# Kernel optimization log

Hardware: AMD Instinct MI355X
Metric: run time of the kernel (lower is better)

The kernel has to match this reference:

```python
import jax, jax.numpy as jnp
import numpy as np

N, M, D, DV = 8192, 8192, 64, 64

def setup_inputs() -> dict:
    key = jax.random.key(0)
    kq, kk, kv = jax.random.split(key, 3)
    Q = jax.random.normal(kq, (N, D), dtype=jnp.float32)
    K = jax.random.normal(kk, (M, D), dtype=jnp.float32)
    V = jax.random.normal(kv, (M, DV), dtype=jnp.float32)
    return {"Q": Q, "K": K, "V": V}

def reference(Q, K, V):
    d = K.shape[-1]
    scores = jnp.einsum('nd,md->nm', Q, K) / jnp.sqrt(jnp.float32(d))  # [N, M]
    attn = jax.nn.softmax(scores, axis=-1)
    return attn @ V  # [N, DV]
```

## Files before the change

### kernel.cpp

```cpp
#include <hip/hip_runtime.h>


#define NQ 8192
#define NK 8192

typedef float f32x4 __attribute__((ext_vector_type(4)));
typedef short short8 __attribute__((ext_vector_type(8)));
union U4 { uint4 u; short8 s; };

#define MFMA16 __builtin_amdgcn_mfma_f32_16x16x32_bf16

__device__ __forceinline__ unsigned pk2(float a, float b) {
    unsigned ua = __builtin_bit_cast(unsigned, a);
    unsigned ub = __builtin_bit_cast(unsigned, b);
    ua = (ua + 0x7FFFu + ((ua >> 16) & 1u)) >> 16;
    ub = (ub + 0x7FFFu + ((ub >> 16) & 1u)) & 0xFFFF0000u;
    return ua | ub;
}

__device__ __forceinline__ unsigned pkt(float a, float b) {
    return __builtin_amdgcn_perm(__builtin_bit_cast(unsigned, b),
                                 __builtin_bit_cast(unsigned, a), 0x07060302u);
}

__global__ __launch_bounds__(256)
void prepass(const float* __restrict__ Kg, const float* __restrict__ Vg,
             uint4* __restrict__ Kb4, uint4* __restrict__ Vt4) {
    __shared__ float ld[64 * 33];
    const int t = threadIdx.x, b = blockIdx.x;

    if (b < 256) {
        const int kl = t >> 3, dg = t & 7;
        const int e = kl & 1, i16 = kl >> 1, h = dg >> 2, q = dg & 3;
        const float* gp = Kg + (size_t)(b * 32 + kl) * 64 + dg * 8;
        float4 f0 = *(const float4*)gp;
        float4 f1 = *(const float4*)(gp + 4);
        uint4 o = make_uint4(pk2(f0.x, f0.y), pk2(f0.z, f0.w),
                             pk2(f1.x, f1.y), pk2(f1.z, f1.w));
        Kb4[(size_t)(b * 4 + e * 2 + h) * 64 + i16 * 4 + q] = o;
    } else {
        const int c = b - 256;
        {
            const int key = t >> 3, dg = t & 7;
            const float* gp = Vg + (size_t)(c * 32 + key) * 64 + dg * 8;
            float4 f0 = *(const float4*)gp;
            float4 f1 = *(const float4*)(gp + 4);
            ld[(dg * 8 + 0) * 33 + key] = f0.x;
            ld[(dg * 8 + 1) * 33 + key] = f0.y;
            ld[(dg * 8 + 2) * 33 + key] = f0.z;
            ld[(dg * 8 + 3) * 33 + key] = f0.w;
            ld[(dg * 8 + 4) * 33 + key] = f1.x;
            ld[(dg * 8 + 5) * 33 + key] = f1.y;
            ld[(dg * 8 + 6) * 33 + key] = f1.z;
            ld[(dg * 8 + 7) * 33 + key] = f1.w;
        }
        __syncthreads();
        {
            const int dim = t >> 2, kq = t & 3;
            const int dt = dim >> 4, i16 = dim & 15;
            float v[8];
            #pragma unroll
            for (int j = 0; j < 8; ++j) v[j] = ld[dim * 33 + kq * 8 + j];
            uint4 o = make_uint4(pk2(v[0], v[1]), pk2(v[2], v[3]),
                                 pk2(v[4], v[5]), pk2(v[6], v[7]));
            Vt4[(size_t)(c * 4 + dt) * 64 + i16 * 4 + kq] = o;
        }
    }
}

__global__ __launch_bounds__(512, 1)
void attn_main(const float* __restrict__ Qg,
               const uint4* __restrict__ Kb4,
               const uint4* __restrict__ Vt4,
               float* __restrict__ Opart,
               float* __restrict__ Lpart) {
    __shared__ uint4 shb4[4160];
    float* sF = (float*)shb4;
    unsigned* shu = (unsigned*)shb4;

    const int t = threadIdx.x, w = t >> 6, lane = t & 63;
    const int q = lane >> 4, i16 = lane & 15;
    const int bid = blockIdx.x;
    const int kh = bid & 1;
    const int rg = bid >> 1;
    const int qb0 = rg * 64;
    const int lsl = i16 * 4 + q;
    const int phase = rg & 15;

    const float SCL = 0.18033688011112042f;
    short8 aq[4][2];
    #pragma unroll
    for (int rt = 0; rt < 4; ++rt) {
        const float* qp = Qg + (size_t)(qb0 + rt * 16 + i16) * 64 + q * 8;
        float4 f0 = *(const float4*)(qp);
        float4 f1 = *(const float4*)(qp + 4);
        U4 u;
        u.u = make_uint4(pk2(f0.x * SCL, f0.y * SCL), pk2(f0.z * SCL, f0.w * SCL),
                         pk2(f1.x * SCL, f1.y * SCL), pk2(f1.z * SCL, f1.w * SCL));
        aq[rt][0] = u.s;
        f0 = *(const float4*)(qp + 32);
        f1 = *(const float4*)(qp + 36);
        u.u = make_uint4(pk2(f0.x * SCL, f0.y * SCL), pk2(f0.z * SCL, f0.w * SCL),
                         pk2(f1.x * SCL, f1.y * SCL), pk2(f1.z * SCL, f1.w * SCL));
        aq[rt][1] = u.s;
    }

    f32x4 acc[4][4];
    float lsum[4][4];
    #pragma unroll
    for (int rt = 0; rt < 4; ++rt) {
        #pragma unroll
        for (int dt = 0; dt < 4; ++dt) { acc[rt][dt][0]=0.f; acc[rt][dt][1]=0.f; acc[rt][dt][2]=0.f; acc[rt][dt][3]=0.f; }
        #pragma unroll
        for (int r = 0; r < 4; ++r) lsum[rt][r] = 0.f;
    }

    const int tpw = ((i16 >> 2) & 1) + 2 * q + 32 * (i16 >> 3);
    const int pp  = i16 & 3;
    const int tpr = (q & 1) + 2 * ((i16 >> 2) & 3) + 8 * (i16 & 3) + 32 * (q >> 1);

    uint4 kfA[4], vfA[4], kfB[4], vfB[4];

#define LOAD_T(TT, KD, VD)                                                           \
    do {                                                                             \
        const int cb = ((kh << 7) + ((((TT) + phase) & 15) * 8 + w)) * 4;            \
        _Pragma("unroll")                                                            \
        for (int eh = 0; eh < 4; ++eh)                                               \
            (KD)[eh] = Kb4[(size_t)(cb + eh) * 64 + lsl];                            \
        _Pragma("unroll")                                                            \
        for (int dt = 0; dt < 4; ++dt)                                               \
            (VD)[dt] = Vt4[(size_t)(cb + dt) * 64 + lsl];                            \
    } while (0)

#define QKEXP(KD, PAR)                                                               \
    do {                                                                             \
        _Pragma("unroll")                                                            \
        for (int rt = 0; rt < 4; ++rt) {                                             \
            f32x4 s0, s1;                                                            \
            s0[0]=-16.f; s0[1]=-16.f; s0[2]=-16.f; s0[3]=-16.f;                      \
            s1[0]=-16.f; s1[1]=-16.f; s1[2]=-16.f; s1[3]=-16.f;                      \
            U4 u0, u1, u2, u3;                                                       \
            u0.u = (KD)[0]; u1.u = (KD)[1]; u2.u = (KD)[2]; u3.u = (KD)[3];          \
            s0 = MFMA16(aq[rt][0], u0.s, s0, 0, 0, 0);                               \
            s0 = MFMA16(aq[rt][1], u1.s, s0, 0, 0, 0);                               \
            s1 = MFMA16(aq[rt][0], u2.s, s1, 0, 0, 0);                               \
            s1 = MFMA16(aq[rt][1], u3.s, s1, 0, 0, 0);                               \
            const int rbase = (((w * 4 + rt) * 2) + (PAR)) * 256;                    \
            _Pragma("unroll")                                                        \
            for (int r = 0; r < 4; ++r) {                                            \
                float p0 = __builtin_amdgcn_exp2f(s0[r]);                            \
                float p1 = __builtin_amdgcn_exp2f(s1[r]);                            \
                lsum[rt][r] += p0;                                                   \
                lsum[rt][r] += p1;                                                   \
                shu[rbase + (tpw + 8 * r) * 4 + pp] = pkt(p0, p1);                   \
            }                                                                        \
        }                                                                            \
    } while (0)

#define PVS(VD, PAR)                                                                 \
    do {                                                                             \
        U4 ap[4];                                                                    \
        _Pragma("unroll")                                                            \
        for (int rt = 0; rt < 4; ++rt)                                               \
            ap[rt].u = shb4[(((w * 4 + rt) * 2) + (PAR)) * 64 + tpr];                \
        _Pragma("unroll")                                                            \
        for (int dt = 0; dt < 4; ++dt) {                                             \
            U4 bv; bv.u = (VD)[dt];                                                  \
            _Pragma("unroll")                                                        \
            for (int rt = 0; rt < 4; ++rt)                                           \
                acc[rt][dt] = MFMA16(ap[rt].s, bv.s, acc[rt][dt], 0, 0, 0);          \
        }                                                                            \
    } while (0)

    LOAD_T(0, kfA, vfA);
    LOAD_T(1, kfB, vfB);
    QKEXP(kfA, 0);
    #pragma unroll 1
    for (int tt = 1; tt < 15; tt += 2) {
        QKEXP(kfB, 1);
        PVS(vfA, 0);
        LOAD_T(tt + 1, kfA, vfA);
        QKEXP(kfA, 0);
        PVS(vfB, 1);
        LOAD_T(tt + 2, kfB, vfB);
        __builtin_amdgcn_sched_barrier(0);
    }
    QKEXP(kfB, 1);
    PVS(vfA, 0);
    PVS(vfB, 1);

    #pragma unroll
    for (int rt = 0; rt < 4; ++rt)
        #pragma unroll
        for (int r = 0; r < 4; ++r) {
            float v = lsum[rt][r];
            v += __shfl_xor(v, 1);
            v += __shfl_xor(v, 2);
            v += __shfl_xor(v, 4);
            v += __shfl_xor(v, 8);
            lsum[rt][r] = v;
        }

    __syncthreads();
    for (int step = 4; step >= 1; step >>= 1) {
        if (w >= step && w < 2 * step) {
            float* base = sF + (w - step) * 4160;
            #pragma unroll
            for (int rt = 0; rt < 4; ++rt) {
                #pragma unroll
                for (int dt = 0; dt < 4; ++dt)
                    #pragma unroll
                    for (int r = 0; r < 4; ++r)
                        base[(rt * 16 + 4 * q + r) * 64 + dt * 16 + i16] = acc[rt][dt][r];
                if (i16 == 0) {
                    #pragma unroll
                    for (int r = 0; r < 4; ++r) base[4096 + rt * 16 + 4 * q + r] = lsum[rt][r];
                }
            }
        }
        __syncthreads();
        if (w < step) {
            const float* base = sF + w * 4160;
            #pragma unroll
            for (int rt = 0; rt < 4; ++rt) {
                #pragma unroll
                for (int dt = 0; dt < 4; ++dt)
                    #pragma unroll
                    for (int r = 0; r < 4; ++r)
                        acc[rt][dt][r] += base[(rt * 16 + 4 * q + r) * 64 + dt * 16 + i16];
                #pragma unroll
                for (int r = 0; r < 4; ++r) lsum[rt][r] += base[4096 + rt * 16 + 4 * q + r];
            }
        }
        __syncthreads();
    }

    if (w == 0) {
        #pragma unroll
        for (int rt = 0; rt < 4; ++rt) {
            #pragma unroll
            for (int dt = 0; dt < 4; ++dt)
                #pragma unroll
                for (int r = 0; r < 4; ++r) {
                    const int row = qb0 + rt * 16 + 4 * q + r;
                    Opart[((size_t)kh * 8192 + row) * 64 + dt * 16 + i16] = acc[rt][dt][r];
                }
            if (i16 == 0) {
                #pragma unroll
                for (int r = 0; r < 4; ++r)
                    Lpart[kh * 8192 + qb0 + rt * 16 + 4 * q + r] = lsum[rt][r];
            }
        }
    }
}

__global__ __launch_bounds__(256)
void merge(const float* __restrict__ Opart, const float* __restrict__ Lpart,
           float* __restrict__ Og) {
    const int idx = blockIdx.x * 256 + threadIdx.x;
    const int row = idx >> 4, seg = idx & 15;
    const float4 a = *(const float4*)(Opart + (size_t)row * 64 + seg * 4);
    const float4 b = *(const float4*)(Opart + ((size_t)8192 + row) * 64 + seg * 4);
    const float inv = 1.0f / (Lpart[row] + Lpart[8192 + row]);
    float4 o;
    o.x = (a.x + b.x) * inv;
    o.y = (a.y + b.y) * inv;
    o.z = (a.z + b.z) * inv;
    o.w = (a.w + b.w) * inv;
    *(float4*)(Og + (size_t)row * 64 + seg * 4) = o;
}

extern "C" void kernel_launch(void* const* d_in, const int* in_sizes, int n_in,
                              void* d_out, int out_size, void* d_ws, size_t ws_size,
                              hipStream_t stream) {
    const float* Q = (const float*)d_in[0];
    const float* K = (const float*)d_in[1];
    const float* V = (const float*)d_in[2];
    float* O = (float*)d_out;
    char* ws = (char*)d_ws;
    uint4* Kb4   = (uint4*)ws;
    uint4* Vt4   = (uint4*)(ws + (1 << 20));
    float* Opart = (float*)(ws + (2 << 20));
    float* Lpart = (float*)(ws + (6 << 20));
    hipLaunchKernelGGL(prepass, dim3(512), dim3(256), 0, stream, K, V, Kb4, Vt4);
    hipLaunchKernelGGL(attn_main, dim3(256), dim3(512), 0, stream, Q, Kb4, Vt4, Opart, Lpart);
    hipLaunchKernelGGL(merge, dim3(512), dim3(256), 0, stream, Opart, Lpart, O);
}
```

Before: 89.11 us.

## Split block warps into row groups and triple-buffer K/V tile loads

Splits the eight warps into two row groups of 32 query rows, each with four key-chunk warps. Each warp now covers 32 key tiles over fewer rows, which halves the Q, accumulator and row-sum registers per warp. It also adds a third K/V register buffer with a six-step unrolled loop, so global loads are issued further ahead of the MFMA work. The cost is more K/V traffic per block, because both row groups load the same keys, plus a smaller two-step shared-memory reduction and more register pressure from the extra buffers.

```diff
diff --git a/kernel.cpp b/kernel.cpp
--- a/kernel.cpp
+++ b/kernel.cpp
@@ -80,18 +80,20 @@
 
     const int t = threadIdx.x, w = t >> 6, lane = t & 63;
     const int q = lane >> 4, i16 = lane & 15;
+    const int rw = w >> 2;
+    const int kc = w & 3;
     const int bid = blockIdx.x;
     const int kh = bid & 1;
     const int rg = bid >> 1;
     const int qb0 = rg * 64;
     const int lsl = i16 * 4 + q;
-    const int phase = rg & 15;
+    const int phase = rg & 31;
 
     const float SCL = 0.18033688011112042f;
-    short8 aq[4][2];
+    short8 aq[2][2];
     #pragma unroll
-    for (int rt = 0; rt < 4; ++rt) {
-        const float* qp = Qg + (size_t)(qb0 + rt * 16 + i16) * 64 + q * 8;
+    for (int rt = 0; rt < 2; ++rt) {
+        const float* qp = Qg + (size_t)(qb0 + rw * 32 + rt * 16 + i16) * 64 + q * 8;
         float4 f0 = *(const float4*)(qp);
         float4 f1 = *(const float4*)(qp + 4);
         U4 u;
@@ -105,10 +107,10 @@
         aq[rt][1] = u.s;
     }
 
-    f32x4 acc[4][4];
-    float lsum[4][4];
+    f32x4 acc[2][4];
+    float lsum[2][4];
     #pragma unroll
-    for (int rt = 0; rt < 4; ++rt) {
+    for (int rt = 0; rt < 2; ++rt) {
         #pragma unroll
         for (int dt = 0; dt < 4; ++dt) { acc[rt][dt][0]=0.f; acc[rt][dt][1]=0.f; acc[rt][dt][2]=0.f; acc[rt][dt][3]=0.f; }
         #pragma unroll
@@ -119,11 +121,11 @@
     const int pp  = i16 & 3;
     const int tpr = (q & 1) + 2 * ((i16 >> 2) & 3) + 8 * (i16 & 3) + 32 * (q >> 1);
 
-    uint4 kfA[4], vfA[4], kfB[4], vfB[4];
+    uint4 kfA[4], vfA[4], kfB[4], vfB[4], kfC[4], vfC[4];
 
 #define LOAD_T(TT, KD, VD)                                                           \
     do {                                                                             \
-        const int cb = ((kh << 7) + ((((TT) + phase) & 15) * 8 + w)) * 4;            \
+        const int cb = ((kh << 7) + ((((TT) + phase) & 31) * 4 + kc)) * 4;           \
         _Pragma("unroll")                                                            \
         for (int eh = 0; eh < 4; ++eh)                                               \
             (KD)[eh] = Kb4[(size_t)(cb + eh) * 64 + lsl];                            \
@@ -135,7 +137,7 @@
 #define QKEXP(KD, PAR)                                                               \
     do {                                                                             \
         _Pragma("unroll")                                                            \
-        for (int rt = 0; rt < 4; ++rt) {                                             \
+        for (int rt = 0; rt < 2; ++rt) {                                             \
             f32x4 s0, s1;                                                            \
             s0[0]=-16.f; s0[1]=-16.f; s0[2]=-16.f; s0[3]=-16.f;                      \
             s1[0]=-16.f; s1[1]=-16.f; s1[2]=-16.f; s1[3]=-16.f;                      \
@@ -145,7 +147,7 @@
             s0 = MFMA16(aq[rt][1], u1.s, s0, 0, 0, 0);                               \
             s1 = MFMA16(aq[rt][0], u2.s, s1, 0, 0, 0);                               \
             s1 = MFMA16(aq[rt][1], u3.s, s1, 0, 0, 0);                               \
-            const int rbase = (((w * 4 + rt) * 2) + (PAR)) * 256;                    \
+            const int rbase = (((w * 2 + rt) * 2) + (PAR)) * 256;                    \
             _Pragma("unroll")                                                        \
             for (int r = 0; r < 4; ++r) {                                            \
                 float p0 = __builtin_amdgcn_exp2f(s0[r]);                            \
@@ -159,30 +161,37 @@
 
 #define PVS(VD, PAR)                                                                 \
     do {                                                                             \
-        U4 ap[4];                                                                    \
-        _Pragma("unroll")                                                            \
-        for (int rt = 0; rt < 4; ++rt)                                               \
-            ap[rt].u = shb4[(((w * 4 + rt) * 2) + (PAR)) * 64 + tpr];                \
+        U4 ap[2];                                                                    \
+        _Pragma("unroll")                                                            \
+        for (int rt = 0; rt < 2; ++rt)                                               \
+            ap[rt].u = shb4[(((w * 2 + rt) * 2) + (PAR)) * 64 + tpr];                \
         _Pragma("unroll")                                                            \
         for (int dt = 0; dt < 4; ++dt) {                                             \
             U4 bv; bv.u = (VD)[dt];                                                  \
             _Pragma("unroll")                                                        \
-            for (int rt = 0; rt < 4; ++rt)                                           \
+            for (int rt = 0; rt < 2; ++rt)                                           \
                 acc[rt][dt] = MFMA16(ap[rt].s, bv.s, acc[rt][dt], 0, 0, 0);          \
         }                                                                            \
     } while (0)
 
     LOAD_T(0, kfA, vfA);
     LOAD_T(1, kfB, vfB);
+    LOAD_T(2, kfC, vfC);
+    __builtin_amdgcn_sched_barrier(0);
     QKEXP(kfA, 0);
     #pragma unroll 1
-    for (int tt = 1; tt < 15; tt += 2) {
-        QKEXP(kfB, 1);
-        PVS(vfA, 0);
-        LOAD_T(tt + 1, kfA, vfA);
-        QKEXP(kfA, 0);
-        PVS(vfB, 1);
-        LOAD_T(tt + 2, kfB, vfB);
+    for (int tt = 1; tt < 31; tt += 6) {
+        QKEXP(kfB, 1); PVS(vfA, 0); LOAD_T(tt + 2, kfA, vfA);
+        __builtin_amdgcn_sched_barrier(0);
+        QKEXP(kfC, 0); PVS(vfB, 1); LOAD_T(tt + 3, kfB, vfB);
+        __builtin_amdgcn_sched_barrier(0);
+        QKEXP(kfA, 1); PVS(vfC, 0); LOAD_T(tt + 4, kfC, vfC);
+        __builtin_amdgcn_sched_barrier(0);
+        QKEXP(kfB, 0); PVS(vfA, 1); LOAD_T(tt + 5, kfA, vfA);
+        __builtin_amdgcn_sched_barrier(0);
+        QKEXP(kfC, 1); PVS(vfB, 0); LOAD_T(tt + 6, kfB, vfB);
+        __builtin_amdgcn_sched_barrier(0);
+        QKEXP(kfA, 0); PVS(vfC, 1); LOAD_T(tt + 7, kfC, vfC);
         __builtin_amdgcn_sched_barrier(0);
     }
     QKEXP(kfB, 1);
@@ -190,7 +199,7 @@
     PVS(vfB, 1);
 
     #pragma unroll
-    for (int rt = 0; rt < 4; ++rt)
+    for (int rt = 0; rt < 2; ++rt)
         #pragma unroll
         for (int r = 0; r < 4; ++r) {
             float v = lsum[rt][r];
@@ -202,11 +211,11 @@
         }
 
     __syncthreads();
-    for (int step = 4; step >= 1; step >>= 1) {
-        if (w >= step && w < 2 * step) {
-            float* base = sF + (w - step) * 4160;
-            #pragma unroll
-            for (int rt = 0; rt < 4; ++rt) {
+    for (int step = 2; step >= 1; step >>= 1) {
+        if (kc >= step && kc < 2 * step) {
+            float* base = sF + (w - step) * 2080;
+            #pragma unroll
+            for (int rt = 0; rt < 2; ++rt) {
                 #pragma unroll
                 for (int dt = 0; dt < 4; ++dt)
                     #pragma unroll
@@ -214,41 +223,41 @@
                         base[(rt * 16 + 4 * q + r) * 64 + dt * 16 + i16] = acc[rt][dt][r];
                 if (i16 == 0) {
                     #pragma unroll
-                    for (int r = 0; r < 4; ++r) base[4096 + rt * 16 + 4 * q + r] = lsum[rt][r];
+                    for (int r = 0; r < 4; ++r) base[2048 + rt * 16 + 4 * q + r] = lsum[rt][r];
                 }
             }
         }
         __syncthreads();
-        if (w < step) {
-            const float* base = sF + w * 4160;
-            #pragma unroll
-            for (int rt = 0; rt < 4; ++rt) {
+        if (kc < step) {
+            const float* base = sF + w * 2080;
+            #pragma unroll
+            for (int rt = 0; rt < 2; ++rt) {
                 #pragma unroll
                 for (int dt = 0; dt < 4; ++dt)
                     #pragma unroll
                     for (int r = 0; r < 4; ++r)
                         acc[rt][dt][r] += base[(rt * 16 + 4 * q + r) * 64 + dt * 16 + i16];
                 #pragma unroll
-                for (int r = 0; r < 4; ++r) lsum[rt][r] += base[4096 + rt * 16 + 4 * q + r];
+                for (int r = 0; r < 4; ++r) lsum[rt][r] += base[2048 + rt * 16 + 4 * q + r];
             }
         }
         __syncthreads();
     }
 
-    if (w == 0) {
-        #pragma unroll
-        for (int rt = 0; rt < 4; ++rt) {
+    if (kc == 0) {
+        #pragma unroll
+        for (int rt = 0; rt < 2; ++rt) {
             #pragma unroll
             for (int dt = 0; dt < 4; ++dt)
                 #pragma unroll
                 for (int r = 0; r < 4; ++r) {
-                    const int row = qb0 + rt * 16 + 4 * q + r;
+                    const int row = qb0 + rw * 32 + rt * 16 + 4 * q + r;
                     Opart[((size_t)kh * 8192 + row) * 64 + dt * 16 + i16] = acc[rt][dt][r];
                 }
             if (i16 == 0) {
                 #pragma unroll
                 for (int r = 0; r < 4; ++r)
-                    Lpart[kh * 8192 + qb0 + rt * 16 + 4 * q + r] = lsum[rt][r];
+                    Lpart[kh * 8192 + qb0 + rw * 32 + rt * 16 + 4 * q + r] = lsum[rt][r];
             }
         }
     }
```

After: 99.21 us. 1.11x slower.

## Replicate bf16 K/V per XCD and fully unroll triple-buffered main loop

Applied to the files above, without the earlier changes.

The prepass now writes eight copies of the packed bf16 K and transposed V, and each attention block reads the copy selected by bid&7, presumably so each XCD's L2 serves its own copy. The main loop is fully unrolled with three register buffers instead of two, so tile loads are issued two stages ahead of use. K fragment unpacking is hoisted out of the per-row-tile loop. The costs are eightfold prepass write traffic and grid size, a larger workspace, and more register pressure from the third buffer.

```diff
diff --git a/kernel.cpp b/kernel.cpp
--- a/kernel.cpp
+++ b/kernel.cpp
@@ -28,18 +28,21 @@
              uint4* __restrict__ Kb4, uint4* __restrict__ Vt4) {
     __shared__ float ld[64 * 33];
     const int t = threadIdx.x, b = blockIdx.x;
-
-    if (b < 256) {
+    const int copy = b & 7, j = b >> 3;
+    uint4* Kc = Kb4 + (size_t)copy * 65536;
+    uint4* Vc = Vt4 + (size_t)copy * 65536;
+
+    if (j < 256) {
         const int kl = t >> 3, dg = t & 7;
         const int e = kl & 1, i16 = kl >> 1, h = dg >> 2, q = dg & 3;
-        const float* gp = Kg + (size_t)(b * 32 + kl) * 64 + dg * 8;
+        const float* gp = Kg + (size_t)(j * 32 + kl) * 64 + dg * 8;
         float4 f0 = *(const float4*)gp;
         float4 f1 = *(const float4*)(gp + 4);
         uint4 o = make_uint4(pk2(f0.x, f0.y), pk2(f0.z, f0.w),
                              pk2(f1.x, f1.y), pk2(f1.z, f1.w));
-        Kb4[(size_t)(b * 4 + e * 2 + h) * 64 + i16 * 4 + q] = o;
+        Kc[(size_t)(j * 4 + e * 2 + h) * 64 + i16 * 4 + q] = o;
     } else {
-        const int c = b - 256;
+        const int c = j - 256;
         {
             const int key = t >> 3, dg = t & 7;
             const float* gp = Vg + (size_t)(c * 32 + key) * 64 + dg * 8;
@@ -60,10 +63,10 @@
             const int dt = dim >> 4, i16 = dim & 15;
             float v[8];
             #pragma unroll
-            for (int j = 0; j < 8; ++j) v[j] = ld[dim * 33 + kq * 8 + j];
+            for (int jj = 0; jj < 8; ++jj) v[jj] = ld[dim * 33 + kq * 8 + jj];
             uint4 o = make_uint4(pk2(v[0], v[1]), pk2(v[2], v[3]),
                                  pk2(v[4], v[5]), pk2(v[6], v[7]));
-            Vt4[(size_t)(c * 4 + dt) * 64 + i16 * 4 + kq] = o;
+            Vc[(size_t)(c * 4 + dt) * 64 + i16 * 4 + kq] = o;
         }
     }
 }
@@ -86,6 +89,8 @@
     const int qb0 = rg * 64;
     const int lsl = i16 * 4 + q;
     const int phase = rg & 15;
+    const uint4* Kb = Kb4 + (size_t)(bid & 7) * 65536;
+    const uint4* Vt = Vt4 + (size_t)(bid & 7) * 65536;
 
     const float SCL = 0.18033688011112042f;
     short8 aq[4][2];
@@ -119,28 +124,28 @@
     const int pp  = i16 & 3;
     const int tpr = (q & 1) + 2 * ((i16 >> 2) & 3) + 8 * (i16 & 3) + 32 * (q >> 1);
 
-    uint4 kfA[4], vfA[4], kfB[4], vfB[4];
+    uint4 kf0[4], vf0[4], kf1[4], vf1[4], kf2[4], vf2[4];
 
 #define LOAD_T(TT, KD, VD)                                                           \
     do {                                                                             \
         const int cb = ((kh << 7) + ((((TT) + phase) & 15) * 8 + w)) * 4;            \
         _Pragma("unroll")                                                            \
         for (int eh = 0; eh < 4; ++eh)                                               \
-            (KD)[eh] = Kb4[(size_t)(cb + eh) * 64 + lsl];                            \
+            (KD)[eh] = Kb[(size_t)(cb + eh) * 64 + lsl];                             \
         _Pragma("unroll")                                                            \
         for (int dt = 0; dt < 4; ++dt)                                               \
-            (VD)[dt] = Vt4[(size_t)(cb + dt) * 64 + lsl];                            \
+            (VD)[dt] = Vt[(size_t)(cb + dt) * 64 + lsl];                             \
     } while (0)
 
 #define QKEXP(KD, PAR)                                                               \
     do {                                                                             \
+        U4 u0, u1, u2, u3;                                                           \
+        u0.u = (KD)[0]; u1.u = (KD)[1]; u2.u = (KD)[2]; u3.u = (KD)[3];              \
         _Pragma("unroll")                                                            \
         for (int rt = 0; rt < 4; ++rt) {                                             \
             f32x4 s0, s1;                                                            \
             s0[0]=-16.f; s0[1]=-16.f; s0[2]=-16.f; s0[3]=-16.f;                      \
             s1[0]=-16.f; s1[1]=-16.f; s1[2]=-16.f; s1[3]=-16.f;                      \
-            U4 u0, u1, u2, u3;                                                       \
-            u0.u = (KD)[0]; u1.u = (KD)[1]; u2.u = (KD)[2]; u3.u = (KD)[3];          \
             s0 = MFMA16(aq[rt][0], u0.s, s0, 0, 0, 0);                               \
             s0 = MFMA16(aq[rt][1], u1.s, s0, 0, 0, 0);                               \
             s1 = MFMA16(aq[rt][0], u2.s, s1, 0, 0, 0);                               \
@@ -172,22 +177,27 @@
         }                                                                            \
     } while (0)
 
-    LOAD_T(0, kfA, vfA);
-    LOAD_T(1, kfB, vfB);
-    QKEXP(kfA, 0);
-    #pragma unroll 1
-    for (int tt = 1; tt < 15; tt += 2) {
-        QKEXP(kfB, 1);
-        PVS(vfA, 0);
-        LOAD_T(tt + 1, kfA, vfA);
-        QKEXP(kfA, 0);
-        PVS(vfB, 1);
-        LOAD_T(tt + 2, kfB, vfB);
-        __builtin_amdgcn_sched_barrier(0);
-    }
-    QKEXP(kfB, 1);
-    PVS(vfA, 0);
-    PVS(vfB, 1);
+#define SB __builtin_amdgcn_sched_barrier(0)
+
+    LOAD_T(0, kf0, vf0);
+    LOAD_T(1, kf1, vf1);
+    QKEXP(kf0, 0);                LOAD_T(2,  kf2, vf2); SB;
+    QKEXP(kf1, 1); PVS(vf0, 0);   LOAD_T(3,  kf0, vf0); SB;
+    QKEXP(kf2, 0); PVS(vf1, 1);   LOAD_T(4,  kf1, vf1); SB;
+    QKEXP(kf0, 1); PVS(vf2, 0);   LOAD_T(5,  kf2, vf2); SB;
+    QKEXP(kf1, 0); PVS(vf0, 1);   LOAD_T(6,  kf0, vf0); SB;
+    QKEXP(kf2, 1); PVS(vf1, 0);   LOAD_T(7,  kf1, vf1); SB;
+    QKEXP(kf0, 0); PVS(vf2, 1);   LOAD_T(8,  kf2, vf2); SB;
+    QKEXP(kf1, 1); PVS(vf0, 0);   LOAD_T(9,  kf0, vf0); SB;
+    QKEXP(kf2, 0); PVS(vf1, 1);   LOAD_T(10, kf1, vf1); SB;
+    QKEXP(kf0, 1); PVS(vf2, 0);   LOAD_T(11, kf2, vf2); SB;
+    QKEXP(kf1, 0); PVS(vf0, 1);   LOAD_T(12, kf0, vf0); SB;
+    QKEXP(kf2, 1); PVS(vf1, 0);   LOAD_T(13, kf1, vf1); SB;
+    QKEXP(kf0, 0); PVS(vf2, 1);   LOAD_T(14, kf2, vf2); SB;
+    QKEXP(kf1, 1); PVS(vf0, 0);   LOAD_T(15, kf0, vf0); SB;
+    QKEXP(kf2, 0); PVS(vf1, 1);                         SB;
+    QKEXP(kf0, 1); PVS(vf2, 0);                         SB;
+    PVS(vf0, 1);
 
     #pragma unroll
     for (int rt = 0; rt < 4; ++rt)
@@ -202,6 +212,7 @@
         }
 
     __syncthreads();
+    #pragma unroll 1
     for (int step = 4; step >= 1; step >>= 1) {
         if (w >= step && w < 2 * step) {
             float* base = sF + (w - step) * 4160;
@@ -279,10 +290,10 @@
     float* O = (float*)d_out;
     char* ws = (char*)d_ws;
     uint4* Kb4   = (uint4*)ws;
-    uint4* Vt4   = (uint4*)(ws + (1 << 20));
-    float* Opart = (float*)(ws + (2 << 20));
-    float* Lpart = (float*)(ws + (6 << 20));
-    hipLaunchKernelGGL(prepass, dim3(512), dim3(256), 0, stream, K, V, Kb4, Vt4);
+    uint4* Vt4   = (uint4*)(ws + (8 << 20));
+    float* Opart = (float*)(ws + (16 << 20));
+    float* Lpart = (float*)(ws + (20 << 20));
+    hipLaunchKernelGGL(prepass, dim3(4096), dim3(256), 0, stream, K, V, Kb4, Vt4);
     hipLaunchKernelGGL(attn_main, dim3(256), dim3(512), 0, stream, Q, Kb4, Vt4, Opart, Lpart);
     hipLaunchKernelGGL(merge, dim3(512), dim3(256), 0, stream, Opart, Lpart, O);
 }
```

Measured after the change: 97.82 us. 1.1x slower.
